# Optimization experiments

Hardware: AMD Instinct MI355X
Metric: run time of the kernel (lower is better)

Reference implementation:

```python
import jax, jax.numpy as jnp
import numpy as np

HEADS = 16
HEAD_DIM = 64
EMB = HEADS * HEAD_DIM
MAX_REL = 512
B, L = 4, 1024


def _rel_indices(length_q, length_k):
    # Shaw-style clipped relative distance indices into the embeddings table
    dist = jnp.arange(length_k)[None, :] - jnp.arange(length_q)[:, None]
    return jnp.clip(dist, -MAX_REL, MAX_REL) + MAX_REL  # [Lq, Lk] in [0, 2*MAX_REL]


def setup_inputs() -> dict:
    key = jax.random.key(0)
    ks = jax.random.split(key, 16)
    d = {
        "query": jax.random.normal(ks[0], (B, L, EMB), jnp.float32),
        "key": jax.random.normal(ks[1], (B, L, EMB), jnp.float32),
        "value": jax.random.normal(ks[2], (B, L, EMB), jnp.float32),
        "mask": jnp.ones((B, 1, L, L), jnp.int32),
        # per-head Linear(head_dims, head_dims) weights stored torch-style [out, in]
        "Wq": jax.random.normal(ks[3], (HEAD_DIM, HEAD_DIM), jnp.float32) / np.sqrt(HEAD_DIM),
        "bq": jax.random.normal(ks[4], (HEAD_DIM,), jnp.float32) * 0.02,
        "Wk": jax.random.normal(ks[5], (HEAD_DIM, HEAD_DIM), jnp.float32) / np.sqrt(HEAD_DIM),
        "bk": jax.random.normal(ks[6], (HEAD_DIM,), jnp.float32) * 0.02,
        "Wv": jax.random.normal(ks[7], (HEAD_DIM, HEAD_DIM), jnp.float32) / np.sqrt(HEAD_DIM),
        "bv": jax.random.normal(ks[8], (HEAD_DIM,), jnp.float32) * 0.02,
        "Wfc": jax.random.normal(ks[9], (EMB, EMB), jnp.float32) / np.sqrt(EMB),
        "bfc": jax.random.normal(ks[10], (EMB,), jnp.float32) * 0.02,
        "rel_k_table": jax.random.normal(ks[11], (2 * MAX_REL + 1, HEAD_DIM), jnp.float32) * 0.02,
        "rel_v_table": jax.random.normal(ks[12], (2 * MAX_REL + 1, HEAD_DIM), jnp.float32) * 0.02,
    }
    return d


def reference(query, key, value, mask, Wq, bq, Wk, bk, Wv, bv, Wfc, bfc, rel_k_table, rel_v_table):
    b, lq, _ = query.shape
    lk = key.shape[1]
    # split heads then per-head linear projections (torch Linear: x @ W.T + b)
    q = query.reshape(b, lq, HEADS, HEAD_DIM) @ Wq.T + bq
    k = key.reshape(b, lk, HEADS, HEAD_DIM) @ Wk.T + bk
    v = value.reshape(b, lk, HEADS, HEAD_DIM) @ Wv.T + bv

    score = jnp.einsum('bqhd,bkhd->bhqk', q, k)  # [B,H,Lq,Lk]
    score = jnp.where(mask == 0, jnp.float32(-1e20), score)

    idx = _rel_indices(lq, lk)
    a_key = rel_k_table[idx]    # [Lq, Lk, D]
    a_val = rel_v_table[idx]    # [Lq, Lk, D]
    score = score + jnp.einsum('blhd,lrd->bhlr', q, a_key)

    attn = jax.nn.softmax(score / np.sqrt(HEAD_DIM), axis=-1)

    out = jnp.einsum('bhqv,bvhd->bqhd', attn, v)
    # original: einsum('brhl,hld->bhrd', attn[b,h,q,k], a_val[q,k,d]) -> [b,q,h,d]
    out = out + jnp.einsum('bhql,qld->bqhd', attn, a_val)
    out = out.reshape(b, lq, EMB)
    return out @ Wfc.T + bfc
```

## Files before the change

### kernel.cpp

```cpp
#include <hip/hip_runtime.h>
#include <hip/hip_bf16.h>
#include <hip/hip_fp16.h>

#define SEQ 1024
#define HEADS 16
#define HDIM 64
#define EMB 1024
#define TQ 32
#define KQ 256
#define PBA_S 264
#define PBB_S 328
#define RELK_ROWS 1040
#define RELV_S 1064

typedef __bf16 bf16x8 __attribute__((ext_vector_type(8)));
typedef float floatx4 __attribute__((ext_vector_type(4)));
typedef unsigned short u16x4 __attribute__((ext_vector_type(4)));

#if __has_builtin(__builtin_amdgcn_exp2f)
#define EXP2F(x) __builtin_amdgcn_exp2f(x)
#else
#define EXP2F(x) exp2f(x)
#endif

#define QSCALE 0.18033688011112042f
#define PBIAS 6.0f

static __device__ __forceinline__ unsigned short f2bu(float f) {
    __bf16 h = (__bf16)f;
    return __builtin_bit_cast(unsigned short, h);
}
static __device__ __forceinline__ float b2f(unsigned short u) {
    unsigned v = ((unsigned)u) << 16;
    return __builtin_bit_cast(float, v);
}

#define NW (1024 * 1024)
#define NRK (RELK_ROWS * 64)
#define NRV (64 * RELV_S)
#define CONVB ((NW + NRK + NRV) / 256)
#define PREPY 1626
__global__ __launch_bounds__(256) void sa_projprep_kernel(
    const float* __restrict__ qin, const float* __restrict__ kin,
    const float* __restrict__ vin,
    const float* __restrict__ Wq, const float* __restrict__ Wk,
    const float* __restrict__ Wv,
    const float* __restrict__ bq, const float* __restrict__ bk,
    const float* __restrict__ bv_,
    const float* __restrict__ Wfc, const float* __restrict__ relk,
    const float* __restrict__ relv, const int* __restrict__ mask,
    unsigned short* __restrict__ qb, unsigned short* __restrict__ kb,
    unsigned short* __restrict__ vtb,
    unsigned short* __restrict__ wfcb, unsigned short* __restrict__ relkb,
    unsigned short* __restrict__ relvtb, unsigned* __restrict__ part) {
    __shared__ unsigned wok[4];
    const int t = threadIdx.x;
    const int which = blockIdx.y;
    const int bx = blockIdx.x;

    if (bx >= 1024) {
        const int gidx = (bx - 1024) + which * PREPY;
        if (gidx < CONVB) {
            int i = gidx * 256 + t;
            if (i < NW) {
                wfcb[i] = f2bu(Wfc[i]);
            } else if (i < NW + NRK) {
                int j = i - NW;
                int r = j >> 6, d = j & 63;
                relkb[j] = (r <= 1024) ? f2bu(relk[r * 64 + d]) : 0;
            } else {
                int j = i - NW - NRK;
                int d = j / RELV_S, c = j - d * RELV_S;
                relvtb[j] = (c <= 1024) ? f2bu(relv[c * 64 + d]) : 0;
            }
        } else if (gidx < CONVB + 256) {
            const int mb = gidx - CONVB;
            const int b = mb >> 6, chunk = mb & 63;
            const int4* p = (const int4*)(mask + (size_t)b * (SEQ * SEQ) + chunk * 16384);
            int ok = 1;
#pragma unroll
            for (int i = 0; i < 16; ++i) {
                int4 v = p[t + i * 256];
                ok &= (v.x != 0 && v.y != 0 && v.z != 0 && v.w != 0) ? 1 : 0;
            }
            unsigned long long bal = __ballot(ok);
            if ((t & 63) == 0) wok[t >> 6] = (bal == ~0ull) ? 1u : 0u;
            __syncthreads();
            if (t == 0)
                part[b * 64 + chunk] = (wok[0] & wok[1] & wok[2] & wok[3]) ? 0xFFFFFFFFu : 0u;
        }
        return;
    }

    const int w = t >> 6, lane = t & 63;
    const int quad = lane >> 4, l16 = lane & 15;
    const int r0 = (bx >> 2) * 16;
    const int h = (bx & 3) * 4 + w;
    const int bidx = r0 >> 10;
    const int l0 = r0 & 1023;
    const float* x = (which == 0) ? qin : (which == 1) ? kin : vin;
    const float* Wsrc = (which == 0) ? Wq : (which == 1) ? Wk : Wv;
    const float* bias = (which == 0) ? bq : (which == 1) ? bk : bv_;

    bf16x8 wf[4][2];
#pragma unroll
    for (int dt = 0; dt < 4; ++dt)
#pragma unroll
        for (int ks = 0; ks < 2; ++ks) {
            const float* wp = Wsrc + (size_t)(dt * 16 + l16) * 64 + ks * 32 + quad * 8;
            float4 lo = *(const float4*)wp;
            float4 hi = *(const float4*)(wp + 4);
            unsigned short pw[8];
            pw[0] = f2bu(lo.x); pw[1] = f2bu(lo.y); pw[2] = f2bu(lo.z); pw[3] = f2bu(lo.w);
            pw[4] = f2bu(hi.x); pw[5] = f2bu(hi.y); pw[6] = f2bu(hi.z); pw[7] = f2bu(hi.w);
            wf[dt][ks] = *(bf16x8*)pw;
        }

    bf16x8 xf[2];
#pragma unroll
    for (int ks = 0; ks < 2; ++ks) {
        const float* xp = x + (size_t)(r0 + l16) * EMB + h * 64 + ks * 32 + quad * 8;
        float4 lo = *(const float4*)xp;
        float4 hi = *(const float4*)(xp + 4);
        unsigned short px[8];
        px[0] = f2bu(lo.x); px[1] = f2bu(lo.y); px[2] = f2bu(lo.z); px[3] = f2bu(lo.w);
        px[4] = f2bu(hi.x); px[5] = f2bu(hi.y); px[6] = f2bu(hi.z); px[7] = f2bu(hi.w);
        xf[ks] = *(bf16x8*)px;
    }
    const int bh = bidx * HEADS + h;

    if (which < 2) {
        float biasd[4];
#pragma unroll
        for (int dt = 0; dt < 4; ++dt) biasd[dt] = bias[dt * 16 + l16];
        const float sc = (which == 0) ? QSCALE : 1.0f;
        unsigned short* dst = (which == 0) ? qb : kb;
        floatx4 acc[4];
#pragma unroll
        for (int dt = 0; dt < 4; ++dt) acc[dt] = floatx4{0.f, 0.f, 0.f, 0.f};
#pragma unroll
        for (int dt = 0; dt < 4; ++dt)
#pragma unroll
            for (int ks = 0; ks < 2; ++ks)
                acc[dt] = __builtin_amdgcn_mfma_f32_16x16x32_bf16(xf[ks], wf[dt][ks], acc[dt], 0, 0, 0);
#pragma unroll
        for (int dt = 0; dt < 4; ++dt)
#pragma unroll
            for (int i = 0; i < 4; ++i) {
                const int lr = l0 + quad * 4 + i;
                float val = (acc[dt][i] + biasd[dt]) * sc;
                dst[((size_t)bh * SEQ + lr) * 64 + dt * 16 + l16] = f2bu(val);
            }
    } else {
        float biasv[4][4];
#pragma unroll
        for (int dt = 0; dt < 4; ++dt)
#pragma unroll
            for (int i = 0; i < 4; ++i) biasv[dt][i] = bias[dt * 16 + quad * 4 + i];
        floatx4 acc[4];
#pragma unroll
        for (int dt = 0; dt < 4; ++dt) acc[dt] = floatx4{0.f, 0.f, 0.f, 0.f};
#pragma unroll
        for (int dt = 0; dt < 4; ++dt)
#pragma unroll
            for (int ks = 0; ks < 2; ++ks)
                acc[dt] = __builtin_amdgcn_mfma_f32_16x16x32_bf16(wf[dt][ks], xf[ks], acc[dt], 0, 0, 0);
#pragma unroll
        for (int dt = 0; dt < 4; ++dt)
#pragma unroll
            for (int i = 0; i < 4; ++i) {
                const int d = dt * 16 + quad * 4 + i;
                float val = acc[dt][i] + biasv[dt][i];
                vtb[((size_t)bh * 64 + d) * SEQ + l0 + l16] = f2bu(val);
            }
    }
}

__global__ __launch_bounds__(512, 8) void sa_attn_kernel(
    const unsigned short* __restrict__ qb, const unsigned short* __restrict__ kb,
    const unsigned short* __restrict__ vtb, const int* __restrict__ mask,
    const unsigned short* __restrict__ relkb, const unsigned short* __restrict__ relvtb,
    const unsigned* __restrict__ part, __half* __restrict__ Opart,
    float* __restrict__ ms) {
    __shared__ __align__(16) unsigned short PbA[TQ * PBA_S];
    __shared__ __align__(16) unsigned short PbB[TQ * PBB_S];
    __shared__ unsigned sflag;

    const int tid = threadIdx.x;
    const int w = tid >> 6, lane = tid & 63;
    const int quad = lane >> 4, l16 = lane & 15;
    const int bid = (blockIdx.x & 7) * 1024 + (blockIdx.x >> 3);
    const int quarter = bid & 3;
    const int qt = (bid >> 2) & 31;
    const int bh = bid >> 7;
    const int q0 = qt * TQ;
    const int k0 = quarter * KQ;
    const int b = bh >> 4;

    if (tid < 64) {
        unsigned f = part[b * 64 + tid];
        unsigned long long bal = __ballot(f != 0u);
        if (tid == 0) sflag = (bal == ~0ull) ? 1u : 0u;
    }

    const bool clipped = (k0 - (q0 + 31) < -512) || (k0 + 255 - q0 > 512);
    const int cmin = min(512, max(-512, k0 - (q0 + 31))) + 512;
    const int cmax = min(512, max(-512, k0 + 255 - q0)) + 512;
    const int rsb = cmin & ~15;
    const int cb0 = cmin & ~7;

    bf16x8 aq[2][2];
#pragma unroll
    for (int rt = 0; rt < 2; ++rt) {
        const unsigned short* qrow = qb + ((size_t)bh * SEQ + q0 + rt * 16 + l16) * 64;
        aq[rt][0] = *(const bf16x8*)(qrow + quad * 8);
        aq[rt][1] = *(const bf16x8*)(qrow + 32 + quad * 8);
    }

    {
        const int ct_lo = cmin >> 4, ct_hi = cmax >> 4;
        for (int ct = ct_lo + w; ct <= ct_hi; ct += 8) {
            bf16x8 bf0 = *(const bf16x8*)(relkb + (size_t)(ct * 16 + l16) * 64 + quad * 8);
            bf16x8 bf1 = *(const bf16x8*)(relkb + (size_t)(ct * 16 + l16) * 64 + 32 + quad * 8);
            floatx4 r0 = {0.f, 0.f, 0.f, 0.f}, r1 = {0.f, 0.f, 0.f, 0.f};
            r0 = __builtin_amdgcn_mfma_f32_16x16x32_bf16(bf0, aq[0][0], r0, 0, 0, 0);
            r0 = __builtin_amdgcn_mfma_f32_16x16x32_bf16(bf1, aq[0][1], r0, 0, 0, 0);
            r1 = __builtin_amdgcn_mfma_f32_16x16x32_bf16(bf0, aq[1][0], r1, 0, 0, 0);
            r1 = __builtin_amdgcn_mfma_f32_16x16x32_bf16(bf1, aq[1][1], r1, 0, 0, 0);
            const int co = ct * 16 + quad * 4 - rsb;
            u16x4 p0, p1;
#pragma unroll
            for (int i = 0; i < 4; ++i) { p0[i] = f2bu(r0[i]); p1[i] = f2bu(r1[i]); }
            *(u16x4*)&PbB[(size_t)l16 * PBB_S + co] = p0;
            *(u16x4*)&PbB[(size_t)(16 + l16) * PBB_S + co] = p1;
        }
    }
    __syncthreads();
    const bool mfull = (sflag != 0u);

    const int kc = w;
    floatx4 acc[2][2];
#pragma unroll
    for (int rt = 0; rt < 2; ++rt)
#pragma unroll
        for (int tt = 0; tt < 2; ++tt) acc[rt][tt] = floatx4{0.f, 0.f, 0.f, 0.f};
#pragma unroll
    for (int tt = 0; tt < 2; ++tt) {
        const unsigned short* krow = kb + ((size_t)bh * SEQ + k0 + kc * 32 + tt * 16 + l16) * 64;
        bf16x8 kf0 = *(const bf16x8*)(krow + quad * 8);
        bf16x8 kf1 = *(const bf16x8*)(krow + 32 + quad * 8);
        acc[0][tt] = __builtin_amdgcn_mfma_f32_16x16x32_bf16(kf0, aq[0][0], acc[0][tt], 0, 0, 0);
        acc[0][tt] = __builtin_amdgcn_mfma_f32_16x16x32_bf16(kf1, aq[0][1], acc[0][tt], 0, 0, 0);
        acc[1][tt] = __builtin_amdgcn_mfma_f32_16x16x32_bf16(kf0, aq[1][0], acc[1][tt], 0, 0, 0);
        acc[1][tt] = __builtin_amdgcn_mfma_f32_16x16x32_bf16(kf1, aq[1][1], acc[1][tt], 0, 0, 0);
    }
    if (!clipped) {
#pragma unroll
        for (int rt = 0; rt < 2; ++rt) {
            const unsigned short* rsrow = &PbB[(size_t)(rt * 16 + l16) * PBB_S];
            const int cb = k0 + kc * 32 - (q0 + rt * 16 + l16) + 512 - rsb;
#pragma unroll
            for (int tt = 0; tt < 2; ++tt)
#pragma unroll
                for (int i = 0; i < 4; ++i)
                    acc[rt][tt][i] += b2f(rsrow[cb + tt * 16 + quad * 4 + i]);
        }
    } else {
#pragma unroll
        for (int rt = 0; rt < 2; ++rt) {
            const unsigned short* rsrow = &PbB[(size_t)(rt * 16 + l16) * PBB_S];
            const int cb = k0 + kc * 32 - (q0 + rt * 16 + l16) + 512;
#pragma unroll
            for (int tt = 0; tt < 2; ++tt)
#pragma unroll
                for (int i = 0; i < 4; ++i) {
                    const int c = cb + tt * 16 + quad * 4 + i;
                    const int r = min(1024, max(0, c));
                    acc[rt][tt][i] += b2f(rsrow[r - rsb]);
                }
        }
    }
    __syncthreads();

    for (int g = tid; g < TQ * (PBB_S / 8); g += 512) {
        int row = g / (PBB_S / 8), j = g - row * (PBB_S / 8);
        *(uint4*)&PbB[row * PBB_S + j * 8] = make_uint4(0u, 0u, 0u, 0u);
    }
    __syncthreads();

#pragma unroll
    for (int rt = 0; rt < 2; ++rt) {
        const int q = q0 + rt * 16 + l16;
        unsigned short* parow = &PbA[(size_t)(rt * 16 + l16) * PBA_S + kc * 32];
        unsigned short* pbrow = &PbB[(size_t)(rt * 16 + l16) * PBB_S];
        const int cbase = k0 + kc * 32 - q + 512;
        const int* mrow = mask + (size_t)b * (SEQ * SEQ) + (size_t)q * SEQ;
#pragma unroll
        for (int tt = 0; tt < 2; ++tt) {
            u16x4 pk;
            if (mfull) {
#pragma unroll
                for (int i = 0; i < 4; ++i)
                    pk[i] = f2bu(EXP2F(acc[rt][tt][i] - PBIAS));
            } else {
#pragma unroll
                for (int i = 0; i < 4; ++i) {
                    const int k = k0 + kc * 32 + tt * 16 + quad * 4 + i;
                    float s = (mrow[k] == 0) ? -1e20f : acc[rt][tt][i];
                    pk[i] = f2bu(EXP2F(s - PBIAS));
                }
            }
            *(u16x4*)(parow + tt * 16 + quad * 4) = pk;
            const int c0 = cbase + tt * 16 + quad * 4;
            if (!clipped) {
#pragma unroll
                for (int i = 0; i < 4; ++i) pbrow[c0 + i - cb0] = pk[i];
            } else {
#pragma unroll
                for (int i = 0; i < 4; ++i) {
                    const int c = c0 + i;
                    if ((unsigned)(c - 1) < 1023u) pbrow[c - cb0] = pk[i];
                }
            }
        }
    }
    __syncthreads();

    {
        const int rt = w & 1;
        const int dq = w >> 1;
        floatx4 accA = {0.f, 0.f, 0.f, 0.f};
        floatx4 accB = {0.f, 0.f, 0.f, 0.f};
        floatx4 accS = {0.f, 0.f, 0.f, 0.f};
        floatx4 accSI = {0.f, 0.f, 0.f, 0.f};
        unsigned short ob[8];
#pragma unroll
        for (int j = 0; j < 8; ++j) ob[j] = 0x3F80;
        const bf16x8 onesf = *(bf16x8*)ob;
        const unsigned short* vbase = vtb + ((size_t)bh * 64 + dq * 16 + l16) * SEQ + k0;
        const unsigned short* rbase = relvtb + (size_t)(dq * 16 + l16) * RELV_S;
        __builtin_amdgcn_s_setprio(1);
#pragma unroll
        for (int it = 0; it < 8; ++it) {
            const int co = it * 32 + quad * 8;
            bf16x8 ap = *(const bf16x8*)&PbA[(size_t)(rt * 16 + l16) * PBA_S + co];
            bf16x8 bv = *(const bf16x8*)(vbase + co);
            accA = __builtin_amdgcn_mfma_f32_16x16x32_bf16(ap, bv, accA, 0, 0, 0);
            accS = __builtin_amdgcn_mfma_f32_16x16x32_bf16(ap, onesf, accS, 0, 0, 0);
        }
        const int nksB = ((cmax - cb0) >> 5) + 1;
        for (int ks = 0; ks < nksB; ++ks) {
            const int co = ks * 32 + quad * 8;
            bf16x8 ar = *(const bf16x8*)&PbB[(size_t)(rt * 16 + l16) * PBB_S + co];
            bf16x8 br = *(const bf16x8*)(rbase + cb0 + co);
            accB = __builtin_amdgcn_mfma_f32_16x16x32_bf16(ar, br, accB, 0, 0, 0);
            accSI = __builtin_amdgcn_mfma_f32_16x16x32_bf16(ar, onesf, accSI, 0, 0, 0);
        }
        __builtin_amdgcn_s_setprio(0);
        const float rv0 = b2f(rbase[0]);
        const float rv1 = b2f(rbase[1024]);
#pragma unroll
        for (int i = 0; i < 4; ++i) {
            const int row = rt * 16 + quad * 4 + i;
            const int q = q0 + row;
            const float tail = accS[i] - accSI[i];
            const float lowS = (q >= k0 + 512) ? tail : 0.f;
            const float highS = (q <= k0 - 257) ? tail : 0.f;
            const int R = bh * SEQ + q;
            float val = accA[i] + accB[i] + lowS * rv0 + highS * rv1;
            Opart[((size_t)R * 4 + quarter) * 64 + dq * 16 + l16] = __float2half(val);
        }
        if (dq == 0 && l16 == 0) {
#pragma unroll
            for (int i = 0; i < 4; ++i) {
                const int row = rt * 16 + quad * 4 + i;
                ms[(size_t)(bh * SEQ + q0 + row) * 4 + quarter] = accS[i];
            }
        }
    }
}

__global__ __launch_bounds__(256) void sa_combine_kernel(
    const __half* __restrict__ Opart, const float* __restrict__ ms,
    unsigned short* __restrict__ aob) {
    const int tid = threadIdx.x;
    const int R = blockIdx.x * 4 + (tid >> 6);
    const int d = tid & 63;
    float4 dn = *(const float4*)&ms[(size_t)R * 4];
    const float inv = 1.f / (dn.x + dn.y + dn.z + dn.w);
    float val = 0.f;
#pragma unroll
    for (int j = 0; j < 4; ++j)
        val += __half2float(Opart[((size_t)R * 4 + j) * 64 + d]);
    val *= inv;
    const int bh = R >> 10, q = R & 1023, b = bh >> 4, h = bh & 15;
    aob[((size_t)b * SEQ + q) * EMB + h * 64 + d] = f2bu(val);
}

__global__ __launch_bounds__(256, 2) void sa_fc_kernel(
    const unsigned short* __restrict__ A, const unsigned short* __restrict__ W,
    const float* __restrict__ bias, float* __restrict__ out) {
    const int t = threadIdx.x;
    const int w = t >> 6, lane = t & 63;
    const int quad = lane >> 4, l16 = lane & 15;
    const int mw = blockIdx.x * 32;
    const int nw = blockIdx.y * 256 + w * 64;

    floatx4 acc[2][4];
#pragma unroll
    for (int mt = 0; mt < 2; ++mt)
#pragma unroll
        for (int j = 0; j < 4; ++j) acc[mt][j] = floatx4{0.f, 0.f, 0.f, 0.f};
    float bj[4];
#pragma unroll
    for (int j = 0; j < 4; ++j) bj[j] = bias[nw + j * 16 + l16];

    for (int ks = 0; ks < 32; ++ks) {
        const int co = ks * 32 + quad * 8;
        bf16x8 af0 = *(const bf16x8*)(A + (size_t)(mw + l16) * EMB + co);
        bf16x8 af1 = *(const bf16x8*)(A + (size_t)(mw + 16 + l16) * EMB + co);
#pragma unroll
        for (int j = 0; j < 4; ++j) {
            bf16x8 bf = *(const bf16x8*)(W + (size_t)(nw + j * 16 + l16) * EMB + co);
            acc[0][j] = __builtin_amdgcn_mfma_f32_16x16x32_bf16(af0, bf, acc[0][j], 0, 0, 0);
            acc[1][j] = __builtin_amdgcn_mfma_f32_16x16x32_bf16(af1, bf, acc[1][j], 0, 0, 0);
        }
    }
#pragma unroll
    for (int mt = 0; mt < 2; ++mt)
#pragma unroll
        for (int j = 0; j < 4; ++j) {
            const int col = nw + j * 16 + l16;
#pragma unroll
            for (int i = 0; i < 4; ++i) {
                const size_t row = mw + mt * 16 + quad * 4 + i;
                out[row * EMB + col] = acc[mt][j][i] + bj[j];
            }
        }
}

extern "C" void kernel_launch(void* const* d_in, const int* in_sizes, int n_in,
                              void* d_out, int out_size, void* d_ws, size_t ws_size,
                              hipStream_t stream) {
    const float* query = (const float*)d_in[0];
    const float* key = (const float*)d_in[1];
    const float* value = (const float*)d_in[2];
    const int* mask = (const int*)d_in[3];
    const float* Wq = (const float*)d_in[4];
    const float* bq = (const float*)d_in[5];
    const float* Wk = (const float*)d_in[6];
    const float* bk = (const float*)d_in[7];
    const float* Wv = (const float*)d_in[8];
    const float* bv = (const float*)d_in[9];
    const float* Wfc = (const float*)d_in[10];
    const float* bfc = (const float*)d_in[11];
    const float* relk = (const float*)d_in[12];
    const float* relv = (const float*)d_in[13];
    float* out = (float*)d_out;

    char* base = (char*)d_ws;
    const size_t MB = (size_t)1 << 20;
    unsigned short* qb = (unsigned short*)(base + 0 * MB);
    unsigned short* aob = qb;
    unsigned short* kb = (unsigned short*)(base + 8 * MB);
    unsigned short* vtb = (unsigned short*)(base + 16 * MB);
    unsigned short* wfcb = (unsigned short*)(base + 24 * MB);
    unsigned short* relkb = (unsigned short*)(base + 26 * MB);
    unsigned short* relvtb = (unsigned short*)(base + 26 * MB + 163840);
    unsigned* part = (unsigned*)(base + 26 * MB + 327680);
    float* ms = (float*)(base + 27 * MB);
    __half* Opart = (__half*)(base + 29 * MB);

    sa_projprep_kernel<<<dim3(1024 + PREPY, 3), 256, 0, stream>>>(
        query, key, value, Wq, Wk, Wv, bq, bk, bv,
        Wfc, relk, relv, mask, qb, kb, vtb, wfcb, relkb, relvtb, part);
    sa_attn_kernel<<<64 * 32 * 4, 512, 0, stream>>>(
        qb, kb, vtb, mask, relkb, relvtb, part, Opart, ms);
    sa_combine_kernel<<<(4 * HEADS * SEQ) / 4, 256, 0, stream>>>(Opart, ms, aob);
    sa_fc_kernel<<<dim3(128, 4), 256, 0, stream>>>(aob, wfcb, bfc, out);
}
```

Measured before the change: 401.7 us.

## Skip redundant row-sum MFMAs for interior tiles and zero only PbB margins

Replaces the full-tile zeroing of the PbB relative-position buffer and its extra barrier with targeted zeroing of only the unused margins in each row, written after the scatter. For tiles whose relative range is not clipped at either table edge, the tail-sum correction is always zero. Those tiles skip the accSI MFMAs, and only the dq==0 waves compute the row-sum accS. The s_setprio hints are removed. This cuts LDS stores, one barrier and MFMA work in the common case, at the cost of more divergent branches and code size.

```diff
diff --git a/kernel.cpp b/kernel.cpp
--- a/kernel.cpp
+++ b/kernel.cpp
@@ -208,6 +208,9 @@
     const int cmax = min(512, max(-512, k0 + 255 - q0)) + 512;
     const int rsb = cmin & ~15;
     const int cb0 = cmin & ~7;
+    const int nksB = ((cmax - cb0) >> 5) + 1;
+    const int RE = cb0 + nksB * 32;
+    const bool interior = (cmin > 0) && (cmax < 1024);
 
     bf16x8 aq[2][2];
 #pragma unroll
@@ -282,12 +285,6 @@
     }
     __syncthreads();
 
-    for (int g = tid; g < TQ * (PBB_S / 8); g += 512) {
-        int row = g / (PBB_S / 8), j = g - row * (PBB_S / 8);
-        *(uint4*)&PbB[row * PBB_S + j * 8] = make_uint4(0u, 0u, 0u, 0u);
-    }
-    __syncthreads();
-
 #pragma unroll
     for (int rt = 0; rt < 2; ++rt) {
         const int q = q0 + rt * 16 + l16;
@@ -322,6 +319,21 @@
                     if ((unsigned)(c - 1) < 1023u) pbrow[c - cb0] = pk[i];
                 }
             }
+        }
+    }
+    {
+#pragma unroll
+        for (int rr = 0; rr < 4; ++rr) {
+            const int row = 4 * w + rr;
+            const int q = q0 + row;
+            const int crow0 = k0 + 512 - q;
+            int st_lo, st_hi1;
+            if (!clipped) { st_lo = crow0; st_hi1 = crow0 + 256; }
+            else { st_lo = max(crow0, 1); st_hi1 = max(st_lo, min(crow0 + 256, 1024)); }
+            unsigned short* pr = &PbB[(size_t)row * PBB_S];
+            const int zl = min(st_lo, RE);
+            for (int x = cb0 + lane; x < zl; x += 64) pr[x - cb0] = 0;
+            for (int x = st_hi1 + lane; x < RE; x += 64) pr[x - cb0] = 0;
         }
     }
     __syncthreads();
@@ -339,31 +351,57 @@
         const bf16x8 onesf = *(bf16x8*)ob;
         const unsigned short* vbase = vtb + ((size_t)bh * 64 + dq * 16 + l16) * SEQ + k0;
         const unsigned short* rbase = relvtb + (size_t)(dq * 16 + l16) * RELV_S;
-        __builtin_amdgcn_s_setprio(1);
-#pragma unroll
-        for (int it = 0; it < 8; ++it) {
-            const int co = it * 32 + quad * 8;
-            bf16x8 ap = *(const bf16x8*)&PbA[(size_t)(rt * 16 + l16) * PBA_S + co];
-            bf16x8 bv = *(const bf16x8*)(vbase + co);
-            accA = __builtin_amdgcn_mfma_f32_16x16x32_bf16(ap, bv, accA, 0, 0, 0);
-            accS = __builtin_amdgcn_mfma_f32_16x16x32_bf16(ap, onesf, accS, 0, 0, 0);
-        }
-        const int nksB = ((cmax - cb0) >> 5) + 1;
-        for (int ks = 0; ks < nksB; ++ks) {
-            const int co = ks * 32 + quad * 8;
-            bf16x8 ar = *(const bf16x8*)&PbB[(size_t)(rt * 16 + l16) * PBB_S + co];
-            bf16x8 br = *(const bf16x8*)(rbase + cb0 + co);
-            accB = __builtin_amdgcn_mfma_f32_16x16x32_bf16(ar, br, accB, 0, 0, 0);
-            accSI = __builtin_amdgcn_mfma_f32_16x16x32_bf16(ar, onesf, accSI, 0, 0, 0);
-        }
-        __builtin_amdgcn_s_setprio(0);
+        const unsigned short* parowF = &PbA[(size_t)(rt * 16 + l16) * PBA_S];
+        const unsigned short* pbrowF = &PbB[(size_t)(rt * 16 + l16) * PBB_S];
+        if (interior) {
+            if (dq == 0) {
+#pragma unroll
+                for (int it = 0; it < 8; ++it) {
+                    const int co = it * 32 + quad * 8;
+                    bf16x8 ap = *(const bf16x8*)(parowF + co);
+                    bf16x8 bv = *(const bf16x8*)(vbase + co);
+                    accA = __builtin_amdgcn_mfma_f32_16x16x32_bf16(ap, bv, accA, 0, 0, 0);
+                    accS = __builtin_amdgcn_mfma_f32_16x16x32_bf16(ap, onesf, accS, 0, 0, 0);
+                }
+            } else {
+#pragma unroll
+                for (int it = 0; it < 8; ++it) {
+                    const int co = it * 32 + quad * 8;
+                    bf16x8 ap = *(const bf16x8*)(parowF + co);
+                    bf16x8 bv = *(const bf16x8*)(vbase + co);
+                    accA = __builtin_amdgcn_mfma_f32_16x16x32_bf16(ap, bv, accA, 0, 0, 0);
+                }
+            }
+            for (int ks = 0; ks < nksB; ++ks) {
+                const int co = ks * 32 + quad * 8;
+                bf16x8 ar = *(const bf16x8*)(pbrowF + co);
+                bf16x8 br = *(const bf16x8*)(rbase + cb0 + co);
+                accB = __builtin_amdgcn_mfma_f32_16x16x32_bf16(ar, br, accB, 0, 0, 0);
+            }
+        } else {
+#pragma unroll
+            for (int it = 0; it < 8; ++it) {
+                const int co = it * 32 + quad * 8;
+                bf16x8 ap = *(const bf16x8*)(parowF + co);
+                bf16x8 bv = *(const bf16x8*)(vbase + co);
+                accA = __builtin_amdgcn_mfma_f32_16x16x32_bf16(ap, bv, accA, 0, 0, 0);
+                accS = __builtin_amdgcn_mfma_f32_16x16x32_bf16(ap, onesf, accS, 0, 0, 0);
+            }
+            for (int ks = 0; ks < nksB; ++ks) {
+                const int co = ks * 32 + quad * 8;
+                bf16x8 ar = *(const bf16x8*)(pbrowF + co);
+                bf16x8 br = *(const bf16x8*)(rbase + cb0 + co);
+                accB = __builtin_amdgcn_mfma_f32_16x16x32_bf16(ar, br, accB, 0, 0, 0);
+                accSI = __builtin_amdgcn_mfma_f32_16x16x32_bf16(ar, onesf, accSI, 0, 0, 0);
+            }
+        }
         const float rv0 = b2f(rbase[0]);
         const float rv1 = b2f(rbase[1024]);
 #pragma unroll
         for (int i = 0; i < 4; ++i) {
             const int row = rt * 16 + quad * 4 + i;
             const int q = q0 + row;
-            const float tail = accS[i] - accSI[i];
+            const float tail = interior ? 0.f : (accS[i] - accSI[i]);
             const float lowS = (q >= k0 + 512) ? tail : 0.f;
             const float highS = (q <= k0 - 257) ? tail : 0.f;
             const int R = bh * SEQ + q;
```

Result: no change. 400.8 us (-0.2%).
